# Kernel optimization log

Hardware: AMD Instinct MI355X
Metric: run time of the kernel (lower is better)

Reference implementation:

```python
import jax, jax.numpy as jnp
import numpy as np

S, X, G = 2048, 2048, 2
INPUT_SIZE = (3, 32, 32)
F = int(np.prod(INPUT_SIZE))


def setup_inputs() -> dict:
    key = jax.random.key(0)
    k1, k2, k3 = jax.random.split(key, 3)
    samples = jax.random.normal(k1, (S,) + INPUT_SIZE, dtype=jnp.float32)
    x = jax.random.normal(k2, (X,) + INPUT_SIZE, dtype=jnp.float32)
    # per-feature std per gradation, kept in [0.1, 1.0) like ranges_std scaling
    std = jax.random.uniform(k3, (G, F), dtype=jnp.float32, minval=0.1, maxval=1.0)
    return {"samples": samples, "x": x, "std": std}


def reference(samples, x, std):
    # samples: [S, C, H, W], x: [X, C, H, W], std: [G, F]
    G_, F_ = std.shape
    s = samples.reshape(samples.shape[0], F_)  # [S, F]
    xf = x.reshape(x.shape[0], F_)             # [X, F]
    w = 1.0 / (std * std)                       # [G, F] precision
    # per-gradation normalizer: -0.5*F*log(2pi) - sum_f log(std)
    const = -0.5 * F_ * jnp.log(2.0 * jnp.pi) - jnp.sum(jnp.log(std), axis=1)  # [G]
    # sum_f -0.5*((s-x)/std)^2 expanded: -0.5*(s^2 w - 2 s w x + x^2 w)
    A = jnp.einsum('sf,gf->gs', s * s, w)        # [G, S]
    C = jnp.einsum('xf,gf->gx', xf * xf, w)      # [G, X]
    B = jnp.einsum('sf,gf,xf->gsx', s, w, xf)    # [G, S, X] cross term
    logits = -0.5 * (A[:, :, None] - 2.0 * B + C[:, None, :]) + const[:, None, None]
    lp = jax.nn.logsumexp(logits, axis=2)        # over x (mixture components)
    lp = jax.nn.logsumexp(lp, axis=0)            # over gradations
    return lp - jnp.log(jnp.float32(x.shape[0] * G_))
```

## Files before the change

### kernel.cpp

```cpp
#include <hip/hip_runtime.h>
#include <math.h>

#define S_N 2048
#define X_N 2048
#define G_N 2
#define F_N 3072

#define TM 128
#define TN 128
#define BK 64
#define ITERS (F_N / BK)
#define NB (X_N / TN)

typedef __bf16 bf16;
typedef __bf16 bf16x4 __attribute__((ext_vector_type(4)));
typedef __bf16 bf16x8 __attribute__((ext_vector_type(8)));
typedef float f32x4 __attribute__((ext_vector_type(4)));
typedef int i32x4 __attribute__((ext_vector_type(4)));

#define LGKM_BARRIER() asm volatile("s_waitcnt lgkmcnt(0)\n\ts_barrier" ::: "memory")

__global__ void k_prep(const float* __restrict__ samples, const float* __restrict__ xin,
                       const float* __restrict__ stdv,
                       bf16* __restrict__ U, bf16* __restrict__ V,
                       float* __restrict__ A, float* __restrict__ C) {
  int r = blockIdx.x;
  int t = threadIdx.x;
  bool isS = (r < S_N);
  const float* src = isS ? (samples + (size_t)r * F_N) : (xin + (size_t)(r - S_N) * F_N);
  float4 row[3];
#pragma unroll
  for (int j = 0; j < 3; ++j) row[j] = ((const float4*)src)[t + j * 256];

  __shared__ float red[4];
  int w = t >> 6, l = t & 63;

  for (int g = 0; g < G_N; ++g) {
    const float4* sd = (const float4*)(stdv + (size_t)g * F_N);
    bf16* dst = isS ? (U + ((size_t)g * S_N + r) * F_N)
                    : (V + ((size_t)g * X_N + (r - S_N)) * F_N);
    float acc = 0.f;
#pragma unroll
    for (int j = 0; j < 3; ++j) {
      float4 d = sd[t + j * 256];
      float u0 = row[j].x * __builtin_amdgcn_rcpf(d.x);
      float u1 = row[j].y * __builtin_amdgcn_rcpf(d.y);
      float u2 = row[j].z * __builtin_amdgcn_rcpf(d.z);
      float u3 = row[j].w * __builtin_amdgcn_rcpf(d.w);
      bf16x4 b;
      b[0] = (bf16)u0; b[1] = (bf16)u1; b[2] = (bf16)u2; b[3] = (bf16)u3;
      float f0 = (float)b[0], f1 = (float)b[1], f2 = (float)b[2], f3 = (float)b[3];
      acc += f0 * f0 + f1 * f1 + f2 * f2 + f3 * f3;
      ((bf16x4*)dst)[t + j * 256] = b;
    }
    for (int o = 32; o; o >>= 1) acc += __shfl_xor(acc, o);
    __syncthreads();
    if (l == 0) red[w] = acc;
    __syncthreads();
    if (t == 0) {
      float tot = red[0] + red[1] + red[2] + red[3];
      if (isS) A[(size_t)g * S_N + r] = tot;
      else     C[(size_t)g * X_N + (r - S_N)] = tot;
    }
  }
}

__global__ __launch_bounds__(256, 2) void k_gemm(const bf16* __restrict__ U, const bf16* __restrict__ V,
                                                 const float* __restrict__ A, const float* __restrict__ C,
                                                 float* __restrict__ pm, float* __restrict__ ps) {
  __shared__ i32x4 ldsA[2][TM * BK / 8];
  __shared__ i32x4 ldsB[2][TN * BK / 8];
  __shared__ float lms[2][TM];
  __shared__ float lss[2][TM];

  int t = threadIdx.x;
  int g = blockIdx.z;
  int bm = blockIdx.y * TM;
  int bn = blockIdx.x * TN;

  const bf16* Ub = U + ((size_t)g * S_N + bm) * F_N;
  const bf16* Vb = V + ((size_t)g * X_N + bn) * F_N;

  int wave = t >> 6, lane = t & 63;
  int wm = wave & 1, wn = wave >> 1;
  int r = lane & 15, q = lane >> 4;
  int fr = (r >> 1) & 7;
  int ck0 = q ^ fr;
  int ck1 = (4 | q) ^ fr;

  int row0 = t >> 3;
  int gcc = (t & 7) ^ ((t >> 4) & 7);
  const bf16* gA[4];
  const bf16* gB[4];
#pragma unroll
  for (int j = 0; j < 4; ++j) {
    gA[j] = Ub + (size_t)(row0 + j * 32) * F_N + gcc * 8;
    gB[j] = Vb + (size_t)(row0 + j * 32) * F_N + gcc * 8;
  }

  f32x4 acc[4][4] = {};
  int abase = (wm * 64 + r) * 8;
  int bbase = (wn * 64 + r) * 8;

  i32x4 sA0[4], sB0[4], sA1[4], sB1[4];

#pragma unroll
  for (int j = 0; j < 4; ++j) {
    sA0[j] = *(const i32x4*)(gA[j]);
    sB0[j] = *(const i32x4*)(gB[j]);
  }
#pragma unroll
  for (int j = 0; j < 4; ++j) {
    sA1[j] = *(const i32x4*)(gA[j] + BK);
    sB1[j] = *(const i32x4*)(gB[j] + BK);
  }
#pragma unroll
  for (int j = 0; j < 4; ++j) {
    ldsA[0][t + j * 256] = sA0[j];
    ldsB[0][t + j * 256] = sB0[j];
  }
  LGKM_BARRIER();

  for (int it = 0; it < ITERS; it += 2) {
    {
      int k2 = it + 2;
      int pk = (k2 < ITERS ? k2 : 0) * BK;
#pragma unroll
      for (int j = 0; j < 4; ++j) {
        sA0[j] = *(const i32x4*)(gA[j] + pk);
        sB0[j] = *(const i32x4*)(gB[j] + pk);
      }
#pragma unroll
      for (int ks = 0; ks < 2; ++ks) {
        int ck = ks ? ck1 : ck0;
        bf16x8 af[4], bfr[4];
#pragma unroll
        for (int mi = 0; mi < 4; ++mi)
          af[mi] = __builtin_bit_cast(bf16x8, ldsA[0][abase + mi * 128 + ck]);
#pragma unroll
        for (int ni = 0; ni < 4; ++ni)
          bfr[ni] = __builtin_bit_cast(bf16x8, ldsB[0][bbase + ni * 128 + ck]);
#pragma unroll
        for (int mi = 0; mi < 4; ++mi)
#pragma unroll
          for (int ni = 0; ni < 4; ++ni)
            acc[mi][ni] = __builtin_amdgcn_mfma_f32_16x16x32_bf16(af[mi], bfr[ni], acc[mi][ni], 0, 0, 0);
      }
#pragma unroll
      for (int j = 0; j < 4; ++j) {
        ldsA[1][t + j * 256] = sA1[j];
        ldsB[1][t + j * 256] = sB1[j];
      }
      LGKM_BARRIER();
    }
    {
      int k3 = it + 3;
      int pk = (k3 < ITERS ? k3 : 0) * BK;
#pragma unroll
      for (int j = 0; j < 4; ++j) {
        sA1[j] = *(const i32x4*)(gA[j] + pk);
        sB1[j] = *(const i32x4*)(gB[j] + pk);
      }
#pragma unroll
      for (int ks = 0; ks < 2; ++ks) {
        int ck = ks ? ck1 : ck0;
        bf16x8 af[4], bfr[4];
#pragma unroll
        for (int mi = 0; mi < 4; ++mi)
          af[mi] = __builtin_bit_cast(bf16x8, ldsA[1][abase + mi * 128 + ck]);
#pragma unroll
        for (int ni = 0; ni < 4; ++ni)
          bfr[ni] = __builtin_bit_cast(bf16x8, ldsB[1][bbase + ni * 128 + ck]);
#pragma unroll
        for (int mi = 0; mi < 4; ++mi)
#pragma unroll
          for (int ni = 0; ni < 4; ++ni)
            acc[mi][ni] = __builtin_amdgcn_mfma_f32_16x16x32_bf16(af[mi], bfr[ni], acc[mi][ni], 0, 0, 0);
      }
#pragma unroll
      for (int j = 0; j < 4; ++j) {
        ldsA[0][t + j * 256] = sA0[j];
        ldsB[0][t + j * 256] = sB0[j];
      }
      LGKM_BARRIER();
    }
  }

  const float* Ap = A + (size_t)g * S_N + bm + wm * 64;
  const float* Cp = C + (size_t)g * X_N + bn + wn * 64;
  float cv[4];
#pragma unroll
  for (int ni = 0; ni < 4; ++ni) cv[ni] = Cp[ni * 16 + r];

  float mloc[4][4], sloc[4][4];
#pragma unroll
  for (int mi = 0; mi < 4; ++mi) {
#pragma unroll
    for (int i = 0; i < 4; ++i) {
      float av = Ap[mi * 16 + q * 4 + i];
      float l0 = acc[mi][0][i] - 0.5f * (av + cv[0]);
      float l1 = acc[mi][1][i] - 0.5f * (av + cv[1]);
      float l2 = acc[mi][2][i] - 0.5f * (av + cv[2]);
      float l3 = acc[mi][3][i] - 0.5f * (av + cv[3]);
      float m = fmaxf(fmaxf(l0, l1), fmaxf(l2, l3));
      m = fmaxf(m, __shfl_xor(m, 1));
      m = fmaxf(m, __shfl_xor(m, 2));
      m = fmaxf(m, __shfl_xor(m, 4));
      m = fmaxf(m, __shfl_xor(m, 8));
      float s = expf(l0 - m) + expf(l1 - m) + expf(l2 - m) + expf(l3 - m);
      s += __shfl_xor(s, 1);
      s += __shfl_xor(s, 2);
      s += __shfl_xor(s, 4);
      s += __shfl_xor(s, 8);
      mloc[mi][i] = m;
      sloc[mi][i] = s;
    }
  }
  if (r == 0) {
#pragma unroll
    for (int mi = 0; mi < 4; ++mi)
#pragma unroll
      for (int i = 0; i < 4; ++i) {
        int rowl = wm * 64 + mi * 16 + q * 4 + i;
        lms[wn][rowl] = mloc[mi][i];
        lss[wn][rowl] = sloc[mi][i];
      }
  }
  __syncthreads();
  if (t < TM) {
    float m0 = lms[0][t], m1 = lms[1][t];
    float s0 = lss[0][t], s1 = lss[1][t];
    float M = fmaxf(m0, m1);
    float S = s0 * expf(m0 - M) + s1 * expf(m1 - M);
    size_t idx = ((size_t)g * NB + blockIdx.x) * S_N + bm + t;
    pm[idx] = M;
    ps[idx] = S;
  }
}

__global__ void k_final(const float* __restrict__ stdv,
                        const float* __restrict__ pm, const float* __restrict__ ps,
                        float* __restrict__ out) {
  int t = threadIdx.x;
  int s = blockIdx.x * 256 + t;

  __shared__ float cgs[G_N];
  __shared__ float red[4];
  for (int g = 0; g < G_N; ++g) {
    float a = 0.f;
    for (int f = t; f < F_N; f += 256) a += logf(stdv[g * F_N + f]);
    for (int o = 32; o; o >>= 1) a += __shfl_xor(a, o);
    __syncthreads();
    if ((t & 63) == 0) red[t >> 6] = a;
    __syncthreads();
    if (t == 0) cgs[g] = -0.5f * (float)F_N * 1.8378770664093453f
                         - (red[0] + red[1] + red[2] + red[3]);
    __syncthreads();
  }
  float cg[G_N];
#pragma unroll
  for (int g = 0; g < G_N; ++g) cg[g] = cgs[g];

  float mv[G_N][NB];
  float M = -INFINITY;
#pragma unroll
  for (int g = 0; g < G_N; ++g)
#pragma unroll
    for (int cb = 0; cb < NB; ++cb) {
      float m = pm[((size_t)g * NB + cb) * S_N + s] + cg[g];
      mv[g][cb] = m;
      M = fmaxf(M, m);
    }
  float T = 0.f;
#pragma unroll
  for (int g = 0; g < G_N; ++g)
#pragma unroll
    for (int cb = 0; cb < NB; ++cb)
      T += ps[((size_t)g * NB + cb) * S_N + s] * expf(mv[g][cb] - M);
  out[s] = M + logf(T) - 8.317766166719343f;
}

extern "C" void kernel_launch(void* const* d_in, const int* in_sizes, int n_in,
                              void* d_out, int out_size, void* d_ws, size_t ws_size,
                              hipStream_t stream) {
  const float* samples = (const float*)d_in[0];
  const float* xin     = (const float*)d_in[1];
  const float* stdv    = (const float*)d_in[2];
  float* out = (float*)d_out;

  char* ws = (char*)d_ws;
  size_t off = 0;
  bf16* U = (bf16*)(ws + off);     off += (size_t)G_N * S_N * F_N * 2;
  bf16* V = (bf16*)(ws + off);     off += (size_t)G_N * X_N * F_N * 2;
  float* A = (float*)(ws + off);   off += (size_t)G_N * S_N * 4;
  float* C = (float*)(ws + off);   off += (size_t)G_N * X_N * 4;
  float* pm = (float*)(ws + off);  off += (size_t)G_N * NB * S_N * 4;
  float* ps = (float*)(ws + off);  off += (size_t)G_N * NB * S_N * 4;

  k_prep<<<dim3(S_N + X_N), dim3(256), 0, stream>>>(samples, xin, stdv, U, V, A, C);
  k_gemm<<<dim3(X_N / TN, S_N / TM, G_N), dim3(256), 0, stream>>>(U, V, A, C, pm, ps);
  k_final<<<dim3(S_N / 256), dim3(256), 0, stream>>>(stdv, pm, ps, out);
}
```

Measured before the change: 165.3 us.

## Load A operand directly from global into registers and shrink prep to one wave

The GEMM no longer stages the A (U) tile through LDS. Each wave loads its MFMA A fragments straight from global memory into registers, one k-step ahead, and keeps only B in double-buffered LDS. This removes the A-side LDS writes and reads and halves the LDS footprint, but each wave now fetches its A rows itself, reading U from global twice as often (the two waves with the same wm both load them), with less coalesced access and more VGPRs. The prep kernel is also rewritten as one 64-thread wave per row, so the row reduction no longer needs shared memory or syncthreads.

```diff
diff --git a/kernel.cpp b/kernel.cpp
--- a/kernel.cpp
+++ b/kernel.cpp
@@ -20,20 +20,18 @@
 
 #define LGKM_BARRIER() asm volatile("s_waitcnt lgkmcnt(0)\n\ts_barrier" ::: "memory")
 
-__global__ void k_prep(const float* __restrict__ samples, const float* __restrict__ xin,
-                       const float* __restrict__ stdv,
-                       bf16* __restrict__ U, bf16* __restrict__ V,
-                       float* __restrict__ A, float* __restrict__ C) {
+__global__ __launch_bounds__(64) void k_prep(const float* __restrict__ samples,
+                                             const float* __restrict__ xin,
+                                             const float* __restrict__ stdv,
+                                             bf16* __restrict__ U, bf16* __restrict__ V,
+                                             float* __restrict__ A, float* __restrict__ C) {
   int r = blockIdx.x;
-  int t = threadIdx.x;
+  int l = threadIdx.x;
   bool isS = (r < S_N);
   const float* src = isS ? (samples + (size_t)r * F_N) : (xin + (size_t)(r - S_N) * F_N);
-  float4 row[3];
-#pragma unroll
-  for (int j = 0; j < 3; ++j) row[j] = ((const float4*)src)[t + j * 256];
-
-  __shared__ float red[4];
-  int w = t >> 6, l = t & 63;
+  float4 row[12];
+#pragma unroll
+  for (int j = 0; j < 12; ++j) row[j] = ((const float4*)src)[l + j * 64];
 
   for (int g = 0; g < G_N; ++g) {
     const float4* sd = (const float4*)(stdv + (size_t)g * F_N);
@@ -41,8 +39,8 @@
                     : (V + ((size_t)g * X_N + (r - S_N)) * F_N);
     float acc = 0.f;
 #pragma unroll
-    for (int j = 0; j < 3; ++j) {
-      float4 d = sd[t + j * 256];
+    for (int j = 0; j < 12; ++j) {
+      float4 d = sd[l + j * 64];
       float u0 = row[j].x * __builtin_amdgcn_rcpf(d.x);
       float u1 = row[j].y * __builtin_amdgcn_rcpf(d.y);
       float u2 = row[j].z * __builtin_amdgcn_rcpf(d.z);
@@ -51,16 +49,12 @@
       b[0] = (bf16)u0; b[1] = (bf16)u1; b[2] = (bf16)u2; b[3] = (bf16)u3;
       float f0 = (float)b[0], f1 = (float)b[1], f2 = (float)b[2], f3 = (float)b[3];
       acc += f0 * f0 + f1 * f1 + f2 * f2 + f3 * f3;
-      ((bf16x4*)dst)[t + j * 256] = b;
+      ((bf16x4*)dst)[l + j * 64] = b;
     }
     for (int o = 32; o; o >>= 1) acc += __shfl_xor(acc, o);
-    __syncthreads();
-    if (l == 0) red[w] = acc;
-    __syncthreads();
-    if (t == 0) {
-      float tot = red[0] + red[1] + red[2] + red[3];
-      if (isS) A[(size_t)g * S_N + r] = tot;
-      else     C[(size_t)g * X_N + (r - S_N)] = tot;
+    if (l == 0) {
+      if (isS) A[(size_t)g * S_N + r] = acc;
+      else     C[(size_t)g * X_N + (r - S_N)] = acc;
     }
   }
 }
@@ -68,7 +62,6 @@
 __global__ __launch_bounds__(256, 2) void k_gemm(const bf16* __restrict__ U, const bf16* __restrict__ V,
                                                  const float* __restrict__ A, const float* __restrict__ C,
                                                  float* __restrict__ pm, float* __restrict__ ps) {
-  __shared__ i32x4 ldsA[2][TM * BK / 8];
   __shared__ i32x4 ldsB[2][TN * BK / 8];
   __shared__ float lms[2][TM];
   __shared__ float lss[2][TM];
@@ -78,7 +71,6 @@
   int bm = blockIdx.y * TM;
   int bn = blockIdx.x * TN;
 
-  const bf16* Ub = U + ((size_t)g * S_N + bm) * F_N;
   const bf16* Vb = V + ((size_t)g * X_N + bn) * F_N;
 
   int wave = t >> 6, lane = t & 63;
@@ -88,100 +80,95 @@
   int ck0 = q ^ fr;
   int ck1 = (4 | q) ^ fr;
 
+  const bf16* pA = U + ((size_t)g * S_N + bm + wm * 64 + r) * F_N + q * 8;
+
   int row0 = t >> 3;
   int gcc = (t & 7) ^ ((t >> 4) & 7);
-  const bf16* gA[4];
   const bf16* gB[4];
 #pragma unroll
-  for (int j = 0; j < 4; ++j) {
-    gA[j] = Ub + (size_t)(row0 + j * 32) * F_N + gcc * 8;
+  for (int j = 0; j < 4; ++j)
     gB[j] = Vb + (size_t)(row0 + j * 32) * F_N + gcc * 8;
-  }
 
   f32x4 acc[4][4] = {};
-  int abase = (wm * 64 + r) * 8;
   int bbase = (wn * 64 + r) * 8;
 
-  i32x4 sA0[4], sB0[4], sA1[4], sB1[4];
-
-#pragma unroll
-  for (int j = 0; j < 4; ++j) {
-    sA0[j] = *(const i32x4*)(gA[j]);
-    sB0[j] = *(const i32x4*)(gB[j]);
-  }
-#pragma unroll
-  for (int j = 0; j < 4; ++j) {
-    sA1[j] = *(const i32x4*)(gA[j] + BK);
-    sB1[j] = *(const i32x4*)(gB[j] + BK);
-  }
-#pragma unroll
-  for (int j = 0; j < 4; ++j) {
-    ldsA[0][t + j * 256] = sA0[j];
-    ldsB[0][t + j * 256] = sB0[j];
-  }
+  i32x4 sB0[4], sB1[4];
+  i32x4 aA0[8], aA1[8];
+
+#pragma unroll
+  for (int j = 0; j < 4; ++j) sB0[j] = *(const i32x4*)(gB[j]);
+#pragma unroll
+  for (int j = 0; j < 4; ++j) sB1[j] = *(const i32x4*)(gB[j] + BK);
+#pragma unroll
+  for (int mi = 0; mi < 4; ++mi)
+#pragma unroll
+    for (int ks = 0; ks < 2; ++ks)
+      aA0[mi * 2 + ks] = *(const i32x4*)(pA + (size_t)(mi * 16) * F_N + ks * 32);
+#pragma unroll
+  for (int j = 0; j < 4; ++j) ldsB[0][t + j * 256] = sB0[j];
   LGKM_BARRIER();
 
   for (int it = 0; it < ITERS; it += 2) {
     {
       int k2 = it + 2;
-      int pk = (k2 < ITERS ? k2 : 0) * BK;
-#pragma unroll
-      for (int j = 0; j < 4; ++j) {
-        sA0[j] = *(const i32x4*)(gA[j] + pk);
-        sB0[j] = *(const i32x4*)(gB[j] + pk);
-      }
+      int pkB = (k2 < ITERS ? k2 : 0) * BK;
+      int pkA = (it + 1 < ITERS ? it + 1 : 0) * BK;
+#pragma unroll
+      for (int j = 0; j < 4; ++j) sB0[j] = *(const i32x4*)(gB[j] + pkB);
+#pragma unroll
+      for (int mi = 0; mi < 4; ++mi)
+#pragma unroll
+        for (int ks = 0; ks < 2; ++ks)
+          aA1[mi * 2 + ks] = *(const i32x4*)(pA + (size_t)(mi * 16) * F_N + pkA + ks * 32);
+
 #pragma unroll
       for (int ks = 0; ks < 2; ++ks) {
         int ck = ks ? ck1 : ck0;
-        bf16x8 af[4], bfr[4];
-#pragma unroll
-        for (int mi = 0; mi < 4; ++mi)
-          af[mi] = __builtin_bit_cast(bf16x8, ldsA[0][abase + mi * 128 + ck]);
+        bf16x8 bfr[4];
 #pragma unroll
         for (int ni = 0; ni < 4; ++ni)
           bfr[ni] = __builtin_bit_cast(bf16x8, ldsB[0][bbase + ni * 128 + ck]);
 #pragma unroll
-        for (int mi = 0; mi < 4; ++mi)
+        for (int mi = 0; mi < 4; ++mi) {
+          bf16x8 af = __builtin_bit_cast(bf16x8, aA0[mi * 2 + ks]);
 #pragma unroll
           for (int ni = 0; ni < 4; ++ni)
-            acc[mi][ni] = __builtin_amdgcn_mfma_f32_16x16x32_bf16(af[mi], bfr[ni], acc[mi][ni], 0, 0, 0);
+            acc[mi][ni] = __builtin_amdgcn_mfma_f32_16x16x32_bf16(af, bfr[ni], acc[mi][ni], 0, 0, 0);
+        }
       }
 #pragma unroll
-      for (int j = 0; j < 4; ++j) {
-        ldsA[1][t + j * 256] = sA1[j];
-        ldsB[1][t + j * 256] = sB1[j];
-      }
+      for (int j = 0; j < 4; ++j) ldsB[1][t + j * 256] = sB1[j];
       LGKM_BARRIER();
     }
     {
       int k3 = it + 3;
-      int pk = (k3 < ITERS ? k3 : 0) * BK;
-#pragma unroll
-      for (int j = 0; j < 4; ++j) {
-        sA1[j] = *(const i32x4*)(gA[j] + pk);
-        sB1[j] = *(const i32x4*)(gB[j] + pk);
-      }
+      int pkB = (k3 < ITERS ? k3 : 0) * BK;
+      int pkA = (it + 2 < ITERS ? it + 2 : 0) * BK;
+#pragma unroll
+      for (int j = 0; j < 4; ++j) sB1[j] = *(const i32x4*)(gB[j] + pkB);
+#pragma unroll
+      for (int mi = 0; mi < 4; ++mi)
+#pragma unroll
+        for (int ks = 0; ks < 2; ++ks)
+          aA0[mi * 2 + ks] = *(const i32x4*)(pA + (size_t)(mi * 16) * F_N + pkA + ks * 32);
+
 #pragma unroll
       for (int ks = 0; ks < 2; ++ks) {
         int ck = ks ? ck1 : ck0;
-        bf16x8 af[4], bfr[4];
-#pragma unroll
-        for (int mi = 0; mi < 4; ++mi)
-          af[mi] = __builtin_bit_cast(bf16x8, ldsA[1][abase + mi * 128 + ck]);
+        bf16x8 bfr[4];
 #pragma unroll
         for (int ni = 0; ni < 4; ++ni)
           bfr[ni] = __builtin_bit_cast(bf16x8, ldsB[1][bbase + ni * 128 + ck]);
 #pragma unroll
-        for (int mi = 0; mi < 4; ++mi)
+        for (int mi = 0; mi < 4; ++mi) {
+          bf16x8 af = __builtin_bit_cast(bf16x8, aA1[mi * 2 + ks]);
 #pragma unroll
           for (int ni = 0; ni < 4; ++ni)
-            acc[mi][ni] = __builtin_amdgcn_mfma_f32_16x16x32_bf16(af[mi], bfr[ni], acc[mi][ni], 0, 0, 0);
+            acc[mi][ni] = __builtin_amdgcn_mfma_f32_16x16x32_bf16(af, bfr[ni], acc[mi][ni], 0, 0, 0);
+        }
       }
 #pragma unroll
-      for (int j = 0; j < 4; ++j) {
-        ldsA[0][t + j * 256] = sA0[j];
-        ldsB[0][t + j * 256] = sB0[j];
-      }
+      for (int j = 0; j < 4; ++j) ldsB[0][t + j * 256] = sB0[j];
       LGKM_BARRIER();
     }
   }
@@ -297,7 +284,7 @@
   float* pm = (float*)(ws + off);  off += (size_t)G_N * NB * S_N * 4;
   float* ps = (float*)(ws + off);  off += (size_t)G_N * NB * S_N * 4;
 
-  k_prep<<<dim3(S_N + X_N), dim3(256), 0, stream>>>(samples, xin, stdv, U, V, A, C);
+  k_prep<<<dim3(S_N + X_N), dim3(64), 0, stream>>>(samples, xin, stdv, U, V, A, C);
   k_gemm<<<dim3(X_N / TN, S_N / TM, G_N), dim3(256), 0, stream>>>(U, V, A, C, pm, ps);
   k_final<<<dim3(S_N / 256), dim3(256), 0, stream>>>(stdv, pm, ps, out);
 }
```

New measurement: 209.9 us. +27.0%, slower.

## Hoist LDS fragment reads before stores and use single-wave prep rows

Applied to the files above, without the earlier changes.

In the GEMM main loop, all LDS fragment loads for both k-substeps are now issued before the next tile's shared-memory stores, and the MFMA chain runs afterwards. This lets the LDS writes overlap the matrix math and frees the reads from the write buffer earlier. The cost is extra register pressure from holding twice as many fragments. Separately, the prep kernel uses one 64-thread wavefront per row with 12 float4 loads per lane, which removes the shared-memory reduction and both __syncthreads.

```diff
diff --git a/kernel.cpp b/kernel.cpp
--- a/kernel.cpp
+++ b/kernel.cpp
@@ -20,20 +20,18 @@
 
 #define LGKM_BARRIER() asm volatile("s_waitcnt lgkmcnt(0)\n\ts_barrier" ::: "memory")
 
-__global__ void k_prep(const float* __restrict__ samples, const float* __restrict__ xin,
-                       const float* __restrict__ stdv,
-                       bf16* __restrict__ U, bf16* __restrict__ V,
-                       float* __restrict__ A, float* __restrict__ C) {
+__global__ __launch_bounds__(64) void k_prep(const float* __restrict__ samples,
+                                             const float* __restrict__ xin,
+                                             const float* __restrict__ stdv,
+                                             bf16* __restrict__ U, bf16* __restrict__ V,
+                                             float* __restrict__ A, float* __restrict__ C) {
   int r = blockIdx.x;
-  int t = threadIdx.x;
+  int l = threadIdx.x;
   bool isS = (r < S_N);
   const float* src = isS ? (samples + (size_t)r * F_N) : (xin + (size_t)(r - S_N) * F_N);
-  float4 row[3];
-#pragma unroll
-  for (int j = 0; j < 3; ++j) row[j] = ((const float4*)src)[t + j * 256];
-
-  __shared__ float red[4];
-  int w = t >> 6, l = t & 63;
+  float4 row[12];
+#pragma unroll
+  for (int j = 0; j < 12; ++j) row[j] = ((const float4*)src)[l + j * 64];
 
   for (int g = 0; g < G_N; ++g) {
     const float4* sd = (const float4*)(stdv + (size_t)g * F_N);
@@ -41,8 +39,8 @@
                     : (V + ((size_t)g * X_N + (r - S_N)) * F_N);
     float acc = 0.f;
 #pragma unroll
-    for (int j = 0; j < 3; ++j) {
-      float4 d = sd[t + j * 256];
+    for (int j = 0; j < 12; ++j) {
+      float4 d = sd[l + j * 64];
       float u0 = row[j].x * __builtin_amdgcn_rcpf(d.x);
       float u1 = row[j].y * __builtin_amdgcn_rcpf(d.y);
       float u2 = row[j].z * __builtin_amdgcn_rcpf(d.z);
@@ -51,16 +49,12 @@
       b[0] = (bf16)u0; b[1] = (bf16)u1; b[2] = (bf16)u2; b[3] = (bf16)u3;
       float f0 = (float)b[0], f1 = (float)b[1], f2 = (float)b[2], f3 = (float)b[3];
       acc += f0 * f0 + f1 * f1 + f2 * f2 + f3 * f3;
-      ((bf16x4*)dst)[t + j * 256] = b;
+      ((bf16x4*)dst)[l + j * 64] = b;
     }
     for (int o = 32; o; o >>= 1) acc += __shfl_xor(acc, o);
-    __syncthreads();
-    if (l == 0) red[w] = acc;
-    __syncthreads();
-    if (t == 0) {
-      float tot = red[0] + red[1] + red[2] + red[3];
-      if (isS) A[(size_t)g * S_N + r] = tot;
-      else     C[(size_t)g * X_N + (r - S_N)] = tot;
+    if (l == 0) {
+      if (isS) A[(size_t)g * S_N + r] = acc;
+      else     C[(size_t)g * X_N + (r - S_N)] = acc;
     }
   }
 }
@@ -130,27 +124,29 @@
         sA0[j] = *(const i32x4*)(gA[j] + pk);
         sB0[j] = *(const i32x4*)(gB[j] + pk);
       }
+      bf16x8 af[2][4], bfr[2][4];
 #pragma unroll
       for (int ks = 0; ks < 2; ++ks) {
         int ck = ks ? ck1 : ck0;
-        bf16x8 af[4], bfr[4];
 #pragma unroll
         for (int mi = 0; mi < 4; ++mi)
-          af[mi] = __builtin_bit_cast(bf16x8, ldsA[0][abase + mi * 128 + ck]);
+          af[ks][mi] = __builtin_bit_cast(bf16x8, ldsA[0][abase + mi * 128 + ck]);
 #pragma unroll
         for (int ni = 0; ni < 4; ++ni)
-          bfr[ni] = __builtin_bit_cast(bf16x8, ldsB[0][bbase + ni * 128 + ck]);
-#pragma unroll
-        for (int mi = 0; mi < 4; ++mi)
-#pragma unroll
-          for (int ni = 0; ni < 4; ++ni)
-            acc[mi][ni] = __builtin_amdgcn_mfma_f32_16x16x32_bf16(af[mi], bfr[ni], acc[mi][ni], 0, 0, 0);
+          bfr[ks][ni] = __builtin_bit_cast(bf16x8, ldsB[0][bbase + ni * 128 + ck]);
       }
 #pragma unroll
       for (int j = 0; j < 4; ++j) {
         ldsA[1][t + j * 256] = sA1[j];
         ldsB[1][t + j * 256] = sB1[j];
       }
+#pragma unroll
+      for (int ks = 0; ks < 2; ++ks)
+#pragma unroll
+        for (int mi = 0; mi < 4; ++mi)
+#pragma unroll
+          for (int ni = 0; ni < 4; ++ni)
+            acc[mi][ni] = __builtin_amdgcn_mfma_f32_16x16x32_bf16(af[ks][mi], bfr[ks][ni], acc[mi][ni], 0, 0, 0);
       LGKM_BARRIER();
     }
     {
@@ -161,27 +157,29 @@
         sA1[j] = *(const i32x4*)(gA[j] + pk);
         sB1[j] = *(const i32x4*)(gB[j] + pk);
       }
+      bf16x8 af[2][4], bfr[2][4];
 #pragma unroll
       for (int ks = 0; ks < 2; ++ks) {
         int ck = ks ? ck1 : ck0;
-        bf16x8 af[4], bfr[4];
 #pragma unroll
         for (int mi = 0; mi < 4; ++mi)
-          af[mi] = __builtin_bit_cast(bf16x8, ldsA[1][abase + mi * 128 + ck]);
+          af[ks][mi] = __builtin_bit_cast(bf16x8, ldsA[1][abase + mi * 128 + ck]);
 #pragma unroll
         for (int ni = 0; ni < 4; ++ni)
-          bfr[ni] = __builtin_bit_cast(bf16x8, ldsB[1][bbase + ni * 128 + ck]);
-#pragma unroll
-        for (int mi = 0; mi < 4; ++mi)
-#pragma unroll
-          for (int ni = 0; ni < 4; ++ni)
-            acc[mi][ni] = __builtin_amdgcn_mfma_f32_16x16x32_bf16(af[mi], bfr[ni], acc[mi][ni], 0, 0, 0);
+          bfr[ks][ni] = __builtin_bit_cast(bf16x8, ldsB[1][bbase + ni * 128 + ck]);
       }
 #pragma unroll
       for (int j = 0; j < 4; ++j) {
         ldsA[0][t + j * 256] = sA0[j];
         ldsB[0][t + j * 256] = sB0[j];
       }
+#pragma unroll
+      for (int ks = 0; ks < 2; ++ks)
+#pragma unroll
+        for (int mi = 0; mi < 4; ++mi)
+#pragma unroll
+          for (int ni = 0; ni < 4; ++ni)
+            acc[mi][ni] = __builtin_amdgcn_mfma_f32_16x16x32_bf16(af[ks][mi], bfr[ks][ni], acc[mi][ni], 0, 0, 0);
       LGKM_BARRIER();
     }
   }
@@ -297,7 +295,7 @@
   float* pm = (float*)(ws + off);  off += (size_t)G_N * NB * S_N * 4;
   float* ps = (float*)(ws + off);  off += (size_t)G_N * NB * S_N * 4;
 
-  k_prep<<<dim3(S_N + X_N), dim3(256), 0, stream>>>(samples, xin, stdv, U, V, A, C);
+  k_prep<<<dim3(S_N + X_N), dim3(64), 0, stream>>>(samples, xin, stdv, U, V, A, C);
   k_gemm<<<dim3(X_N / TN, S_N / TM, G_N), dim3(256), 0, stream>>>(U, V, A, C, pm, ps);
   k_final<<<dim3(S_N / 256), dim3(256), 0, stream>>>(stdv, pm, ps, out);
 }
```

Measured after the change: 166.1 us. About the same (+0.5%).
